# Kernel tuning notes

Hardware: AMD Instinct MI355X
Metric: run time of the kernel (lower is better)

The kernel has to match this reference:

```python
import jax, jax.numpy as jnp
import numpy as np

N = 4096      # nodes
F = 256       # dim_feat
D = 64        # dim_hid == dim_readout
H = 4         # nheads
ALPHA = 0.2   # LeakyReLU negative slope
NEG = jnp.float32(-9e15)


def setup_inputs() -> dict:
    key = jax.random.key(0)
    ks = jax.random.split(key, 6)
    x = jax.random.normal(ks[0], (N, F), jnp.float32)
    adj = jax.random.randint(ks[1], (N, N), 0, 2, jnp.int32)  # dense 0/1 adjacency
    W1 = jax.random.normal(ks[2], (H, F, D), jnp.float32) * (1.414 / (F ** 0.5))
    a1 = jax.random.normal(ks[3], (H, 2 * D), jnp.float32) * 0.1
    W2 = jax.random.normal(ks[4], (H, H * D, D), jnp.float32) * (1.414 / ((H * D) ** 0.5))
    a2 = jax.random.normal(ks[5], (H, 2 * D), jnp.float32) * 0.1
    t = jnp.zeros((), jnp.float32)
    return {"t": t, "x": x, "adj": adj, "W1": W1, "a1": a1, "W2": W2, "a2": a2}


def _gat_layer(x, adj, W, a):
    """Multi-head dense GAT layer; heads vectorized, outputs concatenated.

    The original builds an [N, N, 2D] concat tensor and multiplies by a [2D,1]
    vector; this factorizes exactly as e_ij = leakyrelu(a1.h_i + a2.h_j).
    """
    h = jnp.einsum('nf,hfd->hnd', x, W)                 # [H,N,D]
    f1 = jnp.einsum('hnd,hd->hn', h, a[:, :D])          # a . h_i part
    f2 = jnp.einsum('hnd,hd->hn', h, a[:, D:])          # a . h_j part
    e = jax.nn.leaky_relu(f1[:, :, None] + f2[:, None, :], ALPHA)  # [H,N,N]
    e = jnp.where(adj[None, :, :] > 0, e, NEG)
    att = jax.nn.softmax(e, axis=-1)                    # row-wise softmax
    out = jax.nn.elu(jnp.einsum('hnm,hmd->hnd', att, h))
    n = x.shape[0]
    return out.transpose(1, 0, 2).reshape(n, -1)        # concat heads -> [N, H*D]


def reference(t, x, adj, W1, a1, W2, a2):
    h1 = _gat_layer(x, adj, W1, a1)   # [N, H*D]
    return _gat_layer(h1, adj, W2, a2)  # [N, H*D]
```

## Files before the change

### kernel.cpp

```cpp
#include <hip/hip_runtime.h>
#include <hip/hip_bf16.h>

#define N_NODES 4096
#define DIMC    256
#define NHEADS  4
#define LOG2E   1.44269504f

typedef __attribute__((ext_vector_type(8))) short  short8;
typedef __attribute__((ext_vector_type(4))) short  short4v;
typedef __attribute__((ext_vector_type(4))) float  float4v;

union S8U { short8 v; unsigned int u[4]; };

#if __has_builtin(__builtin_amdgcn_exp2f)
#define EXP2(x) __builtin_amdgcn_exp2f(x)
#else
#define EXP2(x) exp2f(x)
#endif

__device__ inline unsigned short bf16_bits(__hip_bfloat16 b) {
  union { __hip_bfloat16 b; unsigned short u; } cv; cv.b = b; return cv.u;
}

__device__ inline unsigned fenc(float f) {
  unsigned u = __float_as_uint(f);
  return (u & 0x80000000u) ? ~u : (u | 0x80000000u);
}
__device__ inline float fdec(unsigned k) {
  unsigned u = (k & 0x80000000u) ? (k & 0x7FFFFFFFu) : ~k;
  return __uint_as_float(u);
}

__device__ inline size_t packidx(int r, int k) {
  return ((size_t)(r >> 4) * 8 + (k >> 5)) * 512
       + (((k >> 3) & 3) * 16 + (r & 15)) * 8 + (k & 7);
}

__global__ __launch_bounds__(256) void pack_adj_kernel(
    const int* __restrict__ adj, unsigned long long* __restrict__ bits)
{
  int wid  = blockIdx.x * 4 + (threadIdx.x >> 6);
  int lane = threadIdx.x & 63;
  int row  = wid >> 6;
  int w64  = wid & 63;
  int v = adj[(size_t)row * N_NODES + w64 * 64 + lane];
  unsigned long long m = __ballot(v > 0);
  if (lane == 0) bits[row * 64 + w64] = m;
}

__global__ __launch_bounds__(256) void split_pack_kernel(
    const float* __restrict__ in, unsigned short* __restrict__ hi,
    unsigned short* __restrict__ lo)
{
  int g = blockIdx.x * 256 + threadIdx.x;
  int n = g >> 5, kb = (g & 31) * 8;
  const float* ip = in + (size_t)n * DIMC + kb;
  float4v v0 = *reinterpret_cast<const float4v*>(ip);
  float4v v1 = *reinterpret_cast<const float4v*>(ip + 4);
  short8 oh, ol;
#pragma unroll
  for (int i = 0; i < 8; ++i) {
    float f = (i < 4) ? v0[i] : v1[i - 4];
    __hip_bfloat16 hb = __float2bfloat16(f);
    oh[i] = (short)bf16_bits(hb);
    ol[i] = (short)bf16_bits(__float2bfloat16(f - __bfloat162float(hb)));
  }
  size_t idx = packidx(n, kb);
  *reinterpret_cast<short8*>(hi + idx) = oh;
  *reinterpret_cast<short8*>(lo + idx) = ol;
}

__global__ __launch_bounds__(256) void wpack_kernel(
    const float* __restrict__ W1, const float* __restrict__ W2,
    unsigned short* __restrict__ h1, unsigned short* __restrict__ l1,
    unsigned short* __restrict__ h2, unsigned short* __restrict__ l2)
{
  const float* W = blockIdx.y ? W2 : W1;
  unsigned short* hi = blockIdx.y ? h2 : h1;
  unsigned short* lo = blockIdx.y ? l2 : l1;
  int g = blockIdx.x * 256 + threadIdx.x;
  int c = g >> 5, kb = (g & 31) * 8;
  int h = c >> 6, d = c & 63;
  const float* wp = W + (size_t)h * DIMC * 64 + (size_t)kb * 64 + d;
  short8 oh, ol;
#pragma unroll
  for (int i = 0; i < 8; ++i) {
    float f = wp[i * 64];
    __hip_bfloat16 hb = __float2bfloat16(f);
    oh[i] = (short)bf16_bits(hb);
    ol[i] = (short)bf16_bits(__float2bfloat16(f - __bfloat162float(hb)));
  }
  size_t idx = packidx(c, kb);
  *reinterpret_cast<short8*>(hi + idx) = oh;
  *reinterpret_cast<short8*>(lo + idx) = ol;
}

__global__ __launch_bounds__(256) void gemm_kernel(
    const unsigned short* __restrict__ Ah, const unsigned short* __restrict__ Al,
    const unsigned short* __restrict__ Bh, const unsigned short* __restrict__ Bl,
    float* __restrict__ out, unsigned short* __restrict__ Bpack)
{
  __shared__ float tl[32][33];
  int t = threadIdx.x;
  int wv = t >> 6, lane = t & 63, quad = lane >> 4, col = lane & 15;
  int br = blockIdx.x * 32, bc = blockIdx.y * 32;
  int rt = blockIdx.x * 2 + (wv >> 1);
  int ct = blockIdx.y * 2 + (wv & 1);
  int r0 = br + (wv >> 1) * 16;
  int c0 = bc + (wv & 1) * 16;
  float4v acc = {0, 0, 0, 0};
  const unsigned short* ahp = Ah + (size_t)rt * 4096 + lane * 8;
  const unsigned short* alp = Al + (size_t)rt * 4096 + lane * 8;
  const unsigned short* bhp = Bh + (size_t)ct * 4096 + lane * 8;
  const unsigned short* blp = Bl + (size_t)ct * 4096 + lane * 8;
#pragma unroll
  for (int ks = 0; ks < 8; ++ks) {
    short8 ah = *reinterpret_cast<const short8*>(ahp + ks * 512);
    short8 al = *reinterpret_cast<const short8*>(alp + ks * 512);
    short8 bh = *reinterpret_cast<const short8*>(bhp + ks * 512);
    short8 bl = *reinterpret_cast<const short8*>(blp + ks * 512);
    acc = __builtin_amdgcn_mfma_f32_16x16x32_bf16(ah, bh, acc, 0, 0, 0);
    acc = __builtin_amdgcn_mfma_f32_16x16x32_bf16(ah, bl, acc, 0, 0, 0);
    acc = __builtin_amdgcn_mfma_f32_16x16x32_bf16(al, bh, acc, 0, 0, 0);
  }
  int lr = (wv >> 1) * 16 + quad * 4, lc = (wv & 1) * 16 + col;
#pragma unroll
  for (int r = 0; r < 4; ++r) {
    out[(size_t)(r0 + quad * 4 + r) * DIMC + c0 + col] = acc[r];
    tl[lr + r][lc] = acc[r];
  }
  __syncthreads();
  int tr = t >> 3, tc = (t & 7) * 4;
  short4v oh;
#pragma unroll
  for (int k = 0; k < 4; ++k)
    oh[k] = (short)bf16_bits(__float2bfloat16(tl[tc + k][tr]));
  int c = bc + tr;
  int h = c >> 6, d = c & 63, db = d >> 4, colp = d & 15;
  int quadp = tc >> 3, jj = tc & 7;
  size_t fragu = (((size_t)(h * 128 + blockIdx.x) * 4 + db) * 64
                  + quadp * 16 + colp) * 8 + jj;
  *reinterpret_cast<short4v*>(Bpack + fragu) = oh;
}

__global__ __launch_bounds__(256) void fvec_kernel(
    const float* __restrict__ hA, const float* __restrict__ a,
    float* __restrict__ f1L, float* __restrict__ f2L,
    unsigned* __restrict__ f2enc)
{
  __shared__ float bm[4][4];
  int t = threadIdx.x, wv = t >> 6, lane = t & 63;
  int n = blockIdx.x * 4 + wv;
  int h = lane >> 4, d4 = (lane & 15) * 4;
  float4v v = *reinterpret_cast<const float4v*>(hA + (size_t)n * DIMC + lane * 4);
  const float* ah = a + h * 128;
  float s1 = v[0]*ah[d4] + v[1]*ah[d4+1] + v[2]*ah[d4+2] + v[3]*ah[d4+3];
  float s2 = v[0]*ah[64+d4] + v[1]*ah[64+d4+1] + v[2]*ah[64+d4+2] + v[3]*ah[64+d4+3];
#pragma unroll
  for (int o = 8; o >= 1; o >>= 1) {
    s1 += __shfl_xor(s1, o);
    s2 += __shfl_xor(s2, o);
  }
  float s2s = s2 * LOG2E;
  if ((lane & 15) == 0) {
    f1L[h * N_NODES + n] = s1 * LOG2E;
    f2L[h * N_NODES + n] = s2s;
    bm[wv][h] = s2s;
  }
  __syncthreads();
  if (t < 4) {
    float m = fmaxf(fmaxf(bm[0][t], bm[1][t]), fmaxf(bm[2][t], bm[3][t]));
    atomicMax(f2enc + t, fenc(m));
  }
}

__global__ __launch_bounds__(512, 4) void attn_kernel(
    const unsigned short* __restrict__ Bpack,
    const float* __restrict__ f1L, const float* __restrict__ f2L,
    const unsigned* __restrict__ f2enc,
    const unsigned long long* __restrict__ bits64,
    float* __restrict__ outf, unsigned short* __restrict__ outhi,
    unsigned short* __restrict__ outlo)
{
  __shared__ __align__(16) float part[8][32][68];
  unsigned long long* lds_bits =
      reinterpret_cast<unsigned long long*>(&part[0][0][0]);
  int t = threadIdx.x;
  int wv = t >> 6, lane = t & 63, quad = lane >> 4, col = lane & 15;
  int it = blockIdx.x, h = blockIdx.y;
  int i0 = it * 32;
  int irow0 = i0 + col;
  int irow1 = i0 + 16 + col;

  {
    int rr = t >> 4, tt = (t & 15) * 4;
    const unsigned long long* gsrc = bits64 + (size_t)(i0 + rr) * 64 + tt;
    unsigned long long m0 = gsrc[0], m1 = gsrc[1], m2 = gsrc[2], m3 = gsrc[3];
    lds_bits[(tt + 0) * 32 + rr] = m0;
    lds_bits[(tt + 1) * 32 + rr] = m1;
    lds_bits[(tt + 2) * 32 + rr] = m2;
    lds_bits[(tt + 3) * 32 + rr] = m3;
  }

  float f2m = fdec(f2enc[h]);
  float f1i0 = f1L[h * N_NODES + irow0];
  float f1i1 = f1L[h * N_NODES + irow1];
  float s00 = f1i0 + f2m;
  float m0 = fmaxf(s00, 0.2f * s00);
  float f1m0 = f1i0 - m0;
  float cm0 = -0.8f * m0;
  float s01 = f1i1 + f2m;
  float m1 = fmaxf(s01, 0.2f * s01);
  float f1m1 = f1i1 - m1;
  float cm1 = -0.8f * m1;

  const float* f2h = f2L + h * N_NODES;
  const unsigned short* bp =
      Bpack + ((size_t)(h * 128 + wv * 16)) * 4 * 512 + lane * 8;
  int jbase = wv * 512;

  float4v acc0[4] = {{0,0,0,0},{0,0,0,0},{0,0,0,0},{0,0,0,0}};
  float4v acc1[4] = {{0,0,0,0},{0,0,0,0},{0,0,0,0},{0,0,0,0}};
  float4v accl0 = {0, 0, 0, 0}, accl1 = {0, 0, 0, 0};
  S8U ones;
  ones.u[0] = ones.u[1] = ones.u[2] = ones.u[3] = 0x3F803F80u;

  __syncthreads();

  for (int s = 0; s < 16; ++s) {
    int j0 = jbase + s * 32;
    int tg = j0 >> 6;
    unsigned long long wq0 = lds_bits[tg * 32 + col];
    unsigned long long wq1 = lds_bits[tg * 32 + col + 16];
    int sh = (j0 & 32) | (quad * 8);
    unsigned wb0 = (unsigned)(wq0 >> sh);
    unsigned wb1 = (unsigned)(wq1 >> sh);
    const float* fp = f2h + j0 + quad * 8;
    float4v fa = *reinterpret_cast<const float4v*>(fp);
    float4v fb = *reinterpret_cast<const float4v*>(fp + 4);
    const unsigned short* bs = bp + (size_t)s * 2048;
    short8 b0 = *reinterpret_cast<const short8*>(bs);
    short8 b1 = *reinterpret_cast<const short8*>(bs + 512);
    short8 b2 = *reinterpret_cast<const short8*>(bs + 1024);
    short8 b3 = *reinterpret_cast<const short8*>(bs + 1536);
    float w0[8], w1[8];
#pragma unroll
    for (int jj = 0; jj < 8; ++jj) {
      float fv = (jj < 4) ? fa[jj] : fb[jj - 4];
      float sp0 = f1m0 + fv;
      float tb0 = __builtin_fmaf(0.2f, sp0, cm0);
      float e0 = EXP2(fmaxf(sp0, tb0));
      w0[jj] = (wb0 & (1u << jj)) ? e0 : 0.0f;
      float sp1 = f1m1 + fv;
      float tb1 = __builtin_fmaf(0.2f, sp1, cm1);
      float e1 = EXP2(fmaxf(sp1, tb1));
      w1[jj] = (wb1 & (1u << jj)) ? e1 : 0.0f;
    }
    S8U afr0, afr1;
#pragma unroll
    for (int k2 = 0; k2 < 4; ++k2) {
      afr0.u[k2] = __builtin_amdgcn_perm(__float_as_uint(w0[2 * k2 + 1]),
                                         __float_as_uint(w0[2 * k2]),
                                         0x07060302u);
      afr1.u[k2] = __builtin_amdgcn_perm(__float_as_uint(w1[2 * k2 + 1]),
                                         __float_as_uint(w1[2 * k2]),
                                         0x07060302u);
    }
    acc0[0] = __builtin_amdgcn_mfma_f32_16x16x32_bf16(afr0.v, b0, acc0[0], 0, 0, 0);
    acc0[1] = __builtin_amdgcn_mfma_f32_16x16x32_bf16(afr0.v, b1, acc0[1], 0, 0, 0);
    acc0[2] = __builtin_amdgcn_mfma_f32_16x16x32_bf16(afr0.v, b2, acc0[2], 0, 0, 0);
    acc0[3] = __builtin_amdgcn_mfma_f32_16x16x32_bf16(afr0.v, b3, acc0[3], 0, 0, 0);
    accl0   = __builtin_amdgcn_mfma_f32_16x16x32_bf16(afr0.v, ones.v, accl0, 0, 0, 0);
    acc1[0] = __builtin_amdgcn_mfma_f32_16x16x32_bf16(afr1.v, b0, acc1[0], 0, 0, 0);
    acc1[1] = __builtin_amdgcn_mfma_f32_16x16x32_bf16(afr1.v, b1, acc1[1], 0, 0, 0);
    acc1[2] = __builtin_amdgcn_mfma_f32_16x16x32_bf16(afr1.v, b2, acc1[2], 0, 0, 0);
    acc1[3] = __builtin_amdgcn_mfma_f32_16x16x32_bf16(afr1.v, b3, acc1[3], 0, 0, 0);
    accl1   = __builtin_amdgcn_mfma_f32_16x16x32_bf16(afr1.v, ones.v, accl1, 0, 0, 0);
  }

  __syncthreads();

#pragma unroll
  for (int db = 0; db < 4; ++db)
#pragma unroll
    for (int r = 0; r < 4; ++r) {
      part[wv][quad * 4 + r][db * 16 + col] = acc0[db][r];
      part[wv][16 + quad * 4 + r][db * 16 + col] = acc1[db][r];
    }
  if (col == 0) {
#pragma unroll
    for (int r = 0; r < 4; ++r) {
      part[wv][quad * 4 + r][64] = accl0[r];
      part[wv][16 + quad * 4 + r][64] = accl1[r];
    }
  }
  __syncthreads();

  int row = t >> 4, dd = (t & 15) * 4;
  float4v s = {0, 0, 0, 0};
  float l = 0.f;
#pragma unroll
  for (int w2 = 0; w2 < 8; ++w2) {
    float4v pv = *reinterpret_cast<const float4v*>(&part[w2][row][dd]);
    s += pv;
    l += part[w2][row][64];
  }
  float rl = 1.0f / l;
  float o[4];
#pragma unroll
  for (int r = 0; r < 4; ++r) {
    float v = s[r] * rl;
    o[r] = v > 0.f ? v : EXP2(v * LOG2E) - 1.0f;
  }
  int n2 = i0 + row;
  if (outf) {
    size_t oo = (size_t)n2 * DIMC + h * 64 + dd;
    *reinterpret_cast<float4v*>(outf + oo) = {o[0], o[1], o[2], o[3]};
  } else {
    int cg = h * 64 + dd;
    size_t pidx = packidx(n2, cg);
    short4v ohv, olv;
#pragma unroll
    for (int r = 0; r < 4; ++r) {
      __hip_bfloat16 hb = __float2bfloat16(o[r]);
      ohv[r] = (short)bf16_bits(hb);
      olv[r] = (short)bf16_bits(__float2bfloat16(o[r] - __bfloat162float(hb)));
    }
    *reinterpret_cast<short4v*>(outhi + pidx) = ohv;
    *reinterpret_cast<short4v*>(outlo + pidx) = olv;
  }
}

extern "C" void kernel_launch(void* const* d_in, const int* in_sizes, int n_in,
                              void* d_out, int out_size, void* d_ws, size_t ws_size,
                              hipStream_t stream)
{
  const float* x   = (const float*)d_in[1];
  const int*   adj = (const int*)d_in[2];
  const float* W1  = (const float*)d_in[3];
  const float* a1  = (const float*)d_in[4];
  const float* W2  = (const float*)d_in[5];
  const float* a2  = (const float*)d_in[6];

  char* ws = (char*)d_ws;
  size_t off = 0;
  auto alloc = [&](size_t b) { size_t o = off; off = (off + b + 255) & ~255ULL; return o; };
  size_t o_bits = alloc((size_t)N_NODES * 64 * 8);
  size_t o_w1h  = alloc((size_t)DIMC * DIMC * 2);
  size_t o_w1l  = alloc((size_t)DIMC * DIMC * 2);
  size_t o_w2h  = alloc((size_t)DIMC * DIMC * 2);
  size_t o_w2l  = alloc((size_t)DIMC * DIMC * 2);
  size_t o_xh   = alloc((size_t)N_NODES * DIMC * 2);
  size_t o_xl   = alloc((size_t)N_NODES * DIMC * 2);
  size_t o_hA   = alloc((size_t)N_NODES * DIMC * 4);
  size_t o_bp   = alloc((size_t)N_NODES * DIMC * 2);
  size_t o_x2h  = alloc((size_t)N_NODES * DIMC * 2);
  size_t o_x2l  = alloc((size_t)N_NODES * DIMC * 2);
  size_t o_f1   = alloc((size_t)NHEADS * N_NODES * 4);
  size_t o_f2   = alloc((size_t)NHEADS * N_NODES * 4);
  size_t o_fm   = alloc(256);

  unsigned long long* bits = (unsigned long long*)(ws + o_bits);
  unsigned short* w1h = (unsigned short*)(ws + o_w1h);
  unsigned short* w1l = (unsigned short*)(ws + o_w1l);
  unsigned short* w2h = (unsigned short*)(ws + o_w2h);
  unsigned short* w2l = (unsigned short*)(ws + o_w2l);
  unsigned short* xh  = (unsigned short*)(ws + o_xh);
  unsigned short* xl  = (unsigned short*)(ws + o_xl);
  float*          hA  = (float*)(ws + o_hA);
  unsigned short* bpk = (unsigned short*)(ws + o_bp);
  unsigned short* x2h = (unsigned short*)(ws + o_x2h);
  unsigned short* x2l = (unsigned short*)(ws + o_x2l);
  float* f1p = (float*)(ws + o_f1);
  float* f2p = (float*)(ws + o_f2);
  unsigned* fme = (unsigned*)(ws + o_fm);

  hipMemsetAsync(ws + o_fm, 0, 64, stream);
  pack_adj_kernel<<<N_NODES * 64 / 4, 256, 0, stream>>>(adj, bits);
  wpack_kernel<<<dim3(32, 2), 256, 0, stream>>>(W1, W2, w1h, w1l, w2h, w2l);
  split_pack_kernel<<<N_NODES * DIMC / 8 / 256, 256, 0, stream>>>(x, xh, xl);

  auto layer = [&](const unsigned short* xih, const unsigned short* xil,
                   const unsigned short* wth, const unsigned short* wtl,
                   const float* av, unsigned* fmk, float* outf,
                   unsigned short* oh, unsigned short* ol) {
    gemm_kernel<<<dim3(128, 8), 256, 0, stream>>>(xih, xil, wth, wtl, hA, bpk);
    fvec_kernel<<<1024, 256, 0, stream>>>(hA, av, f1p, f2p, fmk);
    attn_kernel<<<dim3(128, 4), 512, 0, stream>>>(bpk, f1p, f2p, fmk, bits,
                                                  outf, oh, ol);
  };

  layer(xh,  xl,  w1h, w1l, a1, fme,     nullptr,        x2h, x2l);
  layer(x2h, x2l, w2h, w2l, a2, fme + 4, (float*)d_out,  nullptr, nullptr);
}
```

Before: 217.6 us.

## Fuse prep kernels, fold attention-vector dots into GEMM, compute f2 max in attn

Merges adjacency packing, x split, W split and the zeroing of the f1/f2 buffers into one prep launch. The GEMM epilogue now computes the per-node a·h dot products with shuffles and atomicAdds, so the fp32 hA store and the separate fvec kernel are removed. Each attention block recomputes the per-head max of f2 with an LDS tree reduction instead of reading a global atomicMax result. This saves launches and hA traffic, but adds atomic contention, a 4096-element reduction in every attention block, and float-atomic summation order nondeterminism.

```diff
diff --git a/kernel.cpp b/kernel.cpp
--- a/kernel.cpp
+++ b/kernel.cpp
@@ -22,91 +22,86 @@
   union { __hip_bfloat16 b; unsigned short u; } cv; cv.b = b; return cv.u;
 }
 
-__device__ inline unsigned fenc(float f) {
-  unsigned u = __float_as_uint(f);
-  return (u & 0x80000000u) ? ~u : (u | 0x80000000u);
-}
-__device__ inline float fdec(unsigned k) {
-  unsigned u = (k & 0x80000000u) ? (k & 0x7FFFFFFFu) : ~k;
-  return __uint_as_float(u);
-}
-
 __device__ inline size_t packidx(int r, int k) {
   return ((size_t)(r >> 4) * 8 + (k >> 5)) * 512
        + (((k >> 3) & 3) * 16 + (r & 15)) * 8 + (k & 7);
 }
 
-__global__ __launch_bounds__(256) void pack_adj_kernel(
-    const int* __restrict__ adj, unsigned long long* __restrict__ bits)
+__global__ __launch_bounds__(256) void prep_kernel(
+    const int* __restrict__ adj, unsigned long long* __restrict__ bits,
+    const float* __restrict__ x,
+    unsigned short* __restrict__ xh, unsigned short* __restrict__ xl,
+    const float* __restrict__ W1, const float* __restrict__ W2,
+    unsigned short* __restrict__ w1h, unsigned short* __restrict__ w1l,
+    unsigned short* __restrict__ w2h, unsigned short* __restrict__ w2l,
+    float* __restrict__ f12zero)
 {
-  int wid  = blockIdx.x * 4 + (threadIdx.x >> 6);
-  int lane = threadIdx.x & 63;
-  int row  = wid >> 6;
-  int w64  = wid & 63;
-  int v = adj[(size_t)row * N_NODES + w64 * 64 + lane];
-  unsigned long long m = __ballot(v > 0);
-  if (lane == 0) bits[row * 64 + w64] = m;
-}
-
-__global__ __launch_bounds__(256) void split_pack_kernel(
-    const float* __restrict__ in, unsigned short* __restrict__ hi,
-    unsigned short* __restrict__ lo)
-{
-  int g = blockIdx.x * 256 + threadIdx.x;
-  int n = g >> 5, kb = (g & 31) * 8;
-  const float* ip = in + (size_t)n * DIMC + kb;
-  float4v v0 = *reinterpret_cast<const float4v*>(ip);
-  float4v v1 = *reinterpret_cast<const float4v*>(ip + 4);
-  short8 oh, ol;
-#pragma unroll
-  for (int i = 0; i < 8; ++i) {
-    float f = (i < 4) ? v0[i] : v1[i - 4];
-    __hip_bfloat16 hb = __float2bfloat16(f);
-    oh[i] = (short)bf16_bits(hb);
-    ol[i] = (short)bf16_bits(__float2bfloat16(f - __bfloat162float(hb)));
-  }
-  size_t idx = packidx(n, kb);
-  *reinterpret_cast<short8*>(hi + idx) = oh;
-  *reinterpret_cast<short8*>(lo + idx) = ol;
-}
-
-__global__ __launch_bounds__(256) void wpack_kernel(
-    const float* __restrict__ W1, const float* __restrict__ W2,
-    unsigned short* __restrict__ h1, unsigned short* __restrict__ l1,
-    unsigned short* __restrict__ h2, unsigned short* __restrict__ l2)
-{
-  const float* W = blockIdx.y ? W2 : W1;
-  unsigned short* hi = blockIdx.y ? h2 : h1;
-  unsigned short* lo = blockIdx.y ? l2 : l1;
-  int g = blockIdx.x * 256 + threadIdx.x;
-  int c = g >> 5, kb = (g & 31) * 8;
-  int h = c >> 6, d = c & 63;
-  const float* wp = W + (size_t)h * DIMC * 64 + (size_t)kb * 64 + d;
-  short8 oh, ol;
-#pragma unroll
-  for (int i = 0; i < 8; ++i) {
-    float f = wp[i * 64];
-    __hip_bfloat16 hb = __float2bfloat16(f);
-    oh[i] = (short)bf16_bits(hb);
-    ol[i] = (short)bf16_bits(__float2bfloat16(f - __bfloat162float(hb)));
-  }
-  size_t idx = packidx(c, kb);
-  *reinterpret_cast<short8*>(hi + idx) = oh;
-  *reinterpret_cast<short8*>(lo + idx) = ol;
+  int b = blockIdx.x, t = threadIdx.x;
+  if (b < 65536) {
+    int wid  = b * 4 + (t >> 6);
+    int lane = t & 63;
+    int row  = wid >> 6;
+    int w64  = wid & 63;
+    int v = adj[(size_t)row * N_NODES + w64 * 64 + lane];
+    unsigned long long m = __ballot(v > 0);
+    if (lane == 0) bits[row * 64 + w64] = m;
+  } else if (b < 66048) {
+    int g = (b - 65536) * 256 + t;
+    int n = g >> 5, kb = (g & 31) * 8;
+    const float* ip = x + (size_t)n * DIMC + kb;
+    float4v v0 = *reinterpret_cast<const float4v*>(ip);
+    float4v v1 = *reinterpret_cast<const float4v*>(ip + 4);
+    short8 oh, ol;
+#pragma unroll
+    for (int i = 0; i < 8; ++i) {
+      float f = (i < 4) ? v0[i] : v1[i - 4];
+      __hip_bfloat16 hb = __float2bfloat16(f);
+      oh[i] = (short)bf16_bits(hb);
+      ol[i] = (short)bf16_bits(__float2bfloat16(f - __bfloat162float(hb)));
+    }
+    size_t idx = packidx(n, kb);
+    *reinterpret_cast<short8*>(xh + idx) = oh;
+    *reinterpret_cast<short8*>(xl + idx) = ol;
+  } else if (b < 66112) {
+    int bid = b - 66048;
+    const float* W = (bid >> 5) ? W2 : W1;
+    unsigned short* hi = (bid >> 5) ? w2h : w1h;
+    unsigned short* lo = (bid >> 5) ? w2l : w1l;
+    int g = (bid & 31) * 256 + t;
+    int c = g >> 5, kb = (g & 31) * 8;
+    int h = c >> 6, d = c & 63;
+    const float* wp = W + (size_t)h * DIMC * 64 + (size_t)kb * 64 + d;
+    short8 oh, ol;
+#pragma unroll
+    for (int i = 0; i < 8; ++i) {
+      float f = wp[i * 64];
+      __hip_bfloat16 hb = __float2bfloat16(f);
+      oh[i] = (short)bf16_bits(hb);
+      ol[i] = (short)bf16_bits(__float2bfloat16(f - __bfloat162float(hb)));
+    }
+    size_t idx = packidx(c, kb);
+    *reinterpret_cast<short8*>(hi + idx) = oh;
+    *reinterpret_cast<short8*>(lo + idx) = ol;
+  } else {
+    int z = b - 66112;
+    reinterpret_cast<float4v*>(f12zero)[(size_t)z * 256 + t] = {0, 0, 0, 0};
+  }
 }
 
 __global__ __launch_bounds__(256) void gemm_kernel(
     const unsigned short* __restrict__ Ah, const unsigned short* __restrict__ Al,
     const unsigned short* __restrict__ Bh, const unsigned short* __restrict__ Bl,
-    float* __restrict__ out, unsigned short* __restrict__ Bpack)
+    const float* __restrict__ avec,
+    float* __restrict__ f1L, float* __restrict__ f2L,
+    unsigned short* __restrict__ Bpack)
 {
   __shared__ float tl[32][33];
   int t = threadIdx.x;
   int wv = t >> 6, lane = t & 63, quad = lane >> 4, col = lane & 15;
-  int br = blockIdx.x * 32, bc = blockIdx.y * 32;
+  int bc = blockIdx.y * 32;
   int rt = blockIdx.x * 2 + (wv >> 1);
   int ct = blockIdx.y * 2 + (wv & 1);
-  int r0 = br + (wv >> 1) * 16;
+  int r0 = blockIdx.x * 32 + (wv >> 1) * 16;
   int c0 = bc + (wv & 1) * 16;
   float4v acc = {0, 0, 0, 0};
   const unsigned short* ahp = Ah + (size_t)rt * 4096 + lane * 8;
@@ -123,12 +118,30 @@
     acc = __builtin_amdgcn_mfma_f32_16x16x32_bf16(ah, bl, acc, 0, 0, 0);
     acc = __builtin_amdgcn_mfma_f32_16x16x32_bf16(al, bh, acc, 0, 0, 0);
   }
+
+  int hh = blockIdx.y >> 1;
+  int d0 = (c0 + col) & 63;
+  float av1 = avec[hh * 128 + d0];
+  float av2 = avec[hh * 128 + 64 + d0];
+#pragma unroll
+  for (int r = 0; r < 4; ++r) {
+    float v1 = acc[r] * av1;
+    float v2 = acc[r] * av2;
+#pragma unroll
+    for (int o = 8; o >= 1; o >>= 1) {
+      v1 += __shfl_xor(v1, o);
+      v2 += __shfl_xor(v2, o);
+    }
+    if ((lane & 15) == 0) {
+      int n = r0 + quad * 4 + r;
+      atomicAdd(f1L + hh * N_NODES + n, v1 * LOG2E);
+      atomicAdd(f2L + hh * N_NODES + n, v2 * LOG2E);
+    }
+  }
+
   int lr = (wv >> 1) * 16 + quad * 4, lc = (wv & 1) * 16 + col;
 #pragma unroll
-  for (int r = 0; r < 4; ++r) {
-    out[(size_t)(r0 + quad * 4 + r) * DIMC + c0 + col] = acc[r];
-    tl[lr + r][lc] = acc[r];
-  }
+  for (int r = 0; r < 4; ++r) tl[lr + r][lc] = acc[r];
   __syncthreads();
   int tr = t >> 3, tc = (t & 7) * 4;
   short4v oh;
@@ -143,41 +156,9 @@
   *reinterpret_cast<short4v*>(Bpack + fragu) = oh;
 }
 
-__global__ __launch_bounds__(256) void fvec_kernel(
-    const float* __restrict__ hA, const float* __restrict__ a,
-    float* __restrict__ f1L, float* __restrict__ f2L,
-    unsigned* __restrict__ f2enc)
-{
-  __shared__ float bm[4][4];
-  int t = threadIdx.x, wv = t >> 6, lane = t & 63;
-  int n = blockIdx.x * 4 + wv;
-  int h = lane >> 4, d4 = (lane & 15) * 4;
-  float4v v = *reinterpret_cast<const float4v*>(hA + (size_t)n * DIMC + lane * 4);
-  const float* ah = a + h * 128;
-  float s1 = v[0]*ah[d4] + v[1]*ah[d4+1] + v[2]*ah[d4+2] + v[3]*ah[d4+3];
-  float s2 = v[0]*ah[64+d4] + v[1]*ah[64+d4+1] + v[2]*ah[64+d4+2] + v[3]*ah[64+d4+3];
-#pragma unroll
-  for (int o = 8; o >= 1; o >>= 1) {
-    s1 += __shfl_xor(s1, o);
-    s2 += __shfl_xor(s2, o);
-  }
-  float s2s = s2 * LOG2E;
-  if ((lane & 15) == 0) {
-    f1L[h * N_NODES + n] = s1 * LOG2E;
-    f2L[h * N_NODES + n] = s2s;
-    bm[wv][h] = s2s;
-  }
-  __syncthreads();
-  if (t < 4) {
-    float m = fmaxf(fmaxf(bm[0][t], bm[1][t]), fmaxf(bm[2][t], bm[3][t]));
-    atomicMax(f2enc + t, fenc(m));
-  }
-}
-
 __global__ __launch_bounds__(512, 4) void attn_kernel(
     const unsigned short* __restrict__ Bpack,
     const float* __restrict__ f1L, const float* __restrict__ f2L,
-    const unsigned* __restrict__ f2enc,
     const unsigned long long* __restrict__ bits64,
     float* __restrict__ outf, unsigned short* __restrict__ outhi,
     unsigned short* __restrict__ outlo)
@@ -185,6 +166,7 @@
   __shared__ __align__(16) float part[8][32][68];
   unsigned long long* lds_bits =
       reinterpret_cast<unsigned long long*>(&part[0][0][0]);
+  float* red = reinterpret_cast<float*>(&part[2][0][0]);
   int t = threadIdx.x;
   int wv = t >> 6, lane = t & 63, quad = lane >> 4, col = lane & 15;
   int it = blockIdx.x, h = blockIdx.y;
@@ -202,7 +184,21 @@
     lds_bits[(tt + 3) * 32 + rr] = m3;
   }
 
-  float f2m = fdec(f2enc[h]);
+  const float* f2h = f2L + h * N_NODES;
+  {
+    float4v ma = *reinterpret_cast<const float4v*>(f2h + t * 8);
+    float4v mb = *reinterpret_cast<const float4v*>(f2h + t * 8 + 4);
+    red[t] = fmaxf(fmaxf(fmaxf(ma[0], ma[1]), fmaxf(ma[2], ma[3])),
+                   fmaxf(fmaxf(mb[0], mb[1]), fmaxf(mb[2], mb[3])));
+  }
+  __syncthreads();
+#pragma unroll
+  for (int s2 = 256; s2 >= 1; s2 >>= 1) {
+    if (t < s2) red[t] = fmaxf(red[t], red[t + s2]);
+    __syncthreads();
+  }
+  float f2m = red[0];
+
   float f1i0 = f1L[h * N_NODES + irow0];
   float f1i1 = f1L[h * N_NODES + irow1];
   float s00 = f1i0 + f2m;
@@ -214,7 +210,6 @@
   float f1m1 = f1i1 - m1;
   float cm1 = -0.8f * m1;
 
-  const float* f2h = f2L + h * N_NODES;
   const unsigned short* bp =
       Bpack + ((size_t)(h * 128 + wv * 16)) * 4 * 512 + lane * 8;
   int jbase = wv * 512;
@@ -224,8 +219,6 @@
   float4v accl0 = {0, 0, 0, 0}, accl1 = {0, 0, 0, 0};
   S8U ones;
   ones.u[0] = ones.u[1] = ones.u[2] = ones.u[3] = 0x3F803F80u;
-
-  __syncthreads();
 
   for (int s = 0; s < 16; ++s) {
     int j0 = jbase + s * 32;
@@ -352,13 +345,10 @@
   size_t o_w2l  = alloc((size_t)DIMC * DIMC * 2);
   size_t o_xh   = alloc((size_t)N_NODES * DIMC * 2);
   size_t o_xl   = alloc((size_t)N_NODES * DIMC * 2);
-  size_t o_hA   = alloc((size_t)N_NODES * DIMC * 4);
   size_t o_bp   = alloc((size_t)N_NODES * DIMC * 2);
   size_t o_x2h  = alloc((size_t)N_NODES * DIMC * 2);
   size_t o_x2l  = alloc((size_t)N_NODES * DIMC * 2);
-  size_t o_f1   = alloc((size_t)NHEADS * N_NODES * 4);
-  size_t o_f2   = alloc((size_t)NHEADS * N_NODES * 4);
-  size_t o_fm   = alloc(256);
+  size_t o_f12  = alloc((size_t)4 * NHEADS * N_NODES * 4);
 
   unsigned long long* bits = (unsigned long long*)(ws + o_bits);
   unsigned short* w1h = (unsigned short*)(ws + o_w1h);
@@ -367,29 +357,28 @@
   unsigned short* w2l = (unsigned short*)(ws + o_w2l);
   unsigned short* xh  = (unsigned short*)(ws + o_xh);
   unsigned short* xl  = (unsigned short*)(ws + o_xl);
-  float*          hA  = (float*)(ws + o_hA);
   unsigned short* bpk = (unsigned short*)(ws + o_bp);
   unsigned short* x2h = (unsigned short*)(ws + o_x2h);
   unsigned short* x2l = (unsigned short*)(ws + o_x2l);
-  float* f1p = (float*)(ws + o_f1);
-  float* f2p = (float*)(ws + o_f2);
-  unsigned* fme = (unsigned*)(ws + o_fm);
-
-  hipMemsetAsync(ws + o_fm, 0, 64, stream);
-  pack_adj_kernel<<<N_NODES * 64 / 4, 256, 0, stream>>>(adj, bits);
-  wpack_kernel<<<dim3(32, 2), 256, 0, stream>>>(W1, W2, w1h, w1l, w2h, w2l);
-  split_pack_kernel<<<N_NODES * DIMC / 8 / 256, 256, 0, stream>>>(x, xh, xl);
+  float* f12 = (float*)(ws + o_f12);
+  float* f1a = f12;
+  float* f2a = f12 + NHEADS * N_NODES;
+  float* f1b = f12 + 2 * NHEADS * N_NODES;
+  float* f2b = f12 + 3 * NHEADS * N_NODES;
+
+  prep_kernel<<<66176, 256, 0, stream>>>(adj, bits, x, xh, xl, W1, W2,
+                                         w1h, w1l, w2h, w2l, f12);
 
   auto layer = [&](const unsigned short* xih, const unsigned short* xil,
                    const unsigned short* wth, const unsigned short* wtl,
-                   const float* av, unsigned* fmk, float* outf,
+                   const float* av, float* f1p, float* f2p, float* outf,
                    unsigned short* oh, unsigned short* ol) {
-    gemm_kernel<<<dim3(128, 8), 256, 0, stream>>>(xih, xil, wth, wtl, hA, bpk);
-    fvec_kernel<<<1024, 256, 0, stream>>>(hA, av, f1p, f2p, fmk);
-    attn_kernel<<<dim3(128, 4), 512, 0, stream>>>(bpk, f1p, f2p, fmk, bits,
+    gemm_kernel<<<dim3(128, 8), 256, 0, stream>>>(xih, xil, wth, wtl, av,
+                                                  f1p, f2p, bpk);
+    attn_kernel<<<dim3(128, 4), 512, 0, stream>>>(bpk, f1p, f2p, bits,
                                                   outf, oh, ol);
   };
 
-  layer(xh,  xl,  w1h, w1l, a1, fme,     nullptr,        x2h, x2l);
-  layer(x2h, x2l, w2h, w2l, a2, fme + 4, (float*)d_out,  nullptr, nullptr);
-}
+  layer(xh,  xl,  w1h, w1l, a1, f1a, f2a, nullptr,       x2h, x2l);
+  layer(x2h, x2l, w2h, w2l, a2, f1b, f2b, (float*)d_out, nullptr, nullptr);
+}
```

Measured after the change: 188.2 us, median of 2. 13.5% less time.
